# Kernel optimization log

Measured on AMD Instinct MI355X. Metric: run time of the kernel, lower is better.

## Reference

```python
import jax, jax.numpy as jnp
import numpy as np

B, L = 128, 200
NUM_C, D, M = 10000, 128, 64


def setup_inputs() -> dict:
    key = jax.random.key(0)
    ks = jax.random.split(key, 16)
    n = lambda k, s, sc=0.05: jax.random.normal(k, s, dtype=jnp.float32) * sc
    return {
        "q": jax.random.randint(ks[0], (B, L), 0, NUM_C),
        "r": jax.random.randint(ks[1], (B, L), 0, 2),
        "k_emb": n(ks[2], (NUM_C, D)),
        "v_emb": n(ks[3], (2, D)),
        "Mk": n(ks[4], (M, D), 0.2),   # kaiming_normal_
        "Mv0": n(ks[5], (M, D), 0.2),  # kaiming_normal_
        "f_W": n(ks[6], (D, 2 * D)), "f_b": jnp.zeros((D,), jnp.float32),
        "e_W": n(ks[7], (D, D)), "e_b": jnp.zeros((D,), jnp.float32),
        "a_W": n(ks[8], (D, D)), "a_b": jnp.zeros((D,), jnp.float32),
        "ab_W": n(ks[9], (1, D)), "ab_b": jnp.zeros((1,), jnp.float32),
        "df_W": n(ks[10], (1, D)), "df_b": jnp.zeros((1,), jnp.float32),
    }


def reference(q, r, k_emb, v_emb, Mk, Mv0, f_W, f_b, e_W, e_b, a_W, a_b, ab_W, ab_b, df_W, df_b):
    # Embeddings
    k = k_emb[q]                # [B, L, D] question key embedding
    v = k + v_emb[r]            # [B, L, D] value embedding

    # Attention over memory slots, erase/add gates
    w = jax.nn.softmax(jnp.einsum('bld,md->blm', k, Mk), axis=-1)   # [B, L, M]
    e = jax.nn.sigmoid(jnp.einsum('bld,ed->ble', v, e_W) + e_b)      # erase [B, L, D]
    a = jnp.tanh(jnp.einsum('bld,ed->ble', v, a_W) + a_b)            # add   [B, L, D]

    Mvt0 = jnp.broadcast_to(Mv0[None], (q.shape[0], Mv0.shape[0], Mv0.shape[1]))  # [B, M, D]

    def step(Mvt, inp):
        wt, et, at = inp  # [B,M], [B,D], [B,D]
        # read uses memory BEFORE this timestep's write (Mv[:, :-1] in torch)
        read = jnp.einsum('bm,bmd->bd', wt, Mvt)
        we = wt[:, :, None]
        Mvt_new = Mvt * (1.0 - we * et[:, None, :]) + we * at[:, None, :]
        return Mvt_new, read

    _, reads = jax.lax.scan(
        step, Mvt0,
        (w.transpose(1, 0, 2), e.transpose(1, 0, 2), a.transpose(1, 0, 2)))
    reads = reads.transpose(1, 0, 2)  # [B, L, D]

    f = jnp.tanh(jnp.concatenate([reads, k], axis=-1) @ f_W.T + f_b)  # [B, L, D]
    stu_ability = jnp.tanh(f @ ab_W.T + ab_b)   # [B, L, 1] (dropout is identity in eval)
    que_diff = jnp.tanh(k @ df_W.T + df_b)      # [B, L, 1]
    p = jax.nn.sigmoid(3.0 * stu_ability - que_diff)
    return p.squeeze(-1)  # [B, L]
```

## Files before the change

kernel.cpp:

```cpp
#include <hip/hip_runtime.h>

typedef unsigned short ushort_t;
typedef short bf16x8 __attribute__((ext_vector_type(8)));
typedef float f32x4 __attribute__((ext_vector_type(4)));

#define B_ 128
#define L_ 200
#define D_ 128
#define M_ 64

__device__ __forceinline__ float fast_sigmoid(float x) {
    return 1.f / (1.f + __expf(-x));
}

__device__ __forceinline__ float fast_tanh(float x) {
    float xc = fminf(fmaxf(x, -15.f), 15.f);
    float e = __expf(2.f * xc);
    return (e - 1.f) / (e + 1.f);
}

__device__ __forceinline__ ushort_t f2bf(float f) {
    union { float f; unsigned int u; } x;
    x.f = f;
    unsigned int u = x.u;
    unsigned int r = (u + 0x7FFFu + ((u >> 16) & 1u)) >> 16;
    return (ushort_t)r;
}

__device__ __forceinline__ uint4 pack8(float4 a, float4 b) {
    uint4 u;
    u.x = (unsigned)f2bf(a.x) | ((unsigned)f2bf(a.y) << 16);
    u.y = (unsigned)f2bf(a.z) | ((unsigned)f2bf(a.w) << 16);
    u.z = (unsigned)f2bf(b.x) | ((unsigned)f2bf(b.y) << 16);
    u.w = (unsigned)f2bf(b.z) | ((unsigned)f2bf(b.w) << 16);
    return u;
}

#define F_WQ   0u
#define F_EAQ  1638400u
#define F_FKQ  8192000u
#define F_RD   11468800u
#define F_DIFF 14745600u
#define F_PACK 14771200u
#define WPACK_N 57344
#define FPACK_N 16384

__global__ __launch_bounds__(256) void k_pack(
    const float* __restrict__ Mk, const float* __restrict__ eW,
    const float* __restrict__ aW, const float* __restrict__ fW,
    ushort_t* __restrict__ Wpack, ushort_t* __restrict__ Fpack)
{
    int i = blockIdx.x * 256 + threadIdx.x;
    if (i < WPACK_N) {
        int g = i >> 9, lane = (i >> 3) & 63, j = i & 7;
        int nt = g >> 2, ks = g & 3;
        int col = nt * 16 + (lane & 15);
        int d = ks * 32 + ((lane >> 4) << 3) + j;
        float v;
        if (col < 64)       v = Mk[col * 128 + d];
        else if (col < 192) v = eW[(col - 64) * 128 + d];
        else if (col < 320) v = aW[(col - 192) * 128 + d];
        else                v = fW[(col - 320) * 256 + 128 + d];
        Wpack[i] = f2bf(v);
    } else if (i < WPACK_N + FPACK_N) {
        int e = i - WPACK_N;
        int g = e >> 9, lane = (e >> 3) & 63, j = e & 7;
        int nt = g >> 2, ks = g & 3;
        int col = nt * 16 + (lane & 15);
        int d = ks * 32 + ((lane >> 4) << 3) + j;
        Fpack[e] = f2bf(fW[col * 256 + d]);
    }
}

__device__ __forceinline__ void loadB4(const ushort_t* __restrict__ base,
                                       int nt, int lane, bf16x8* b) {
    const ushort_t* p = base + (nt * 256 + lane) * 8;
    b[0] = *(const bf16x8*)(p);
    b[1] = *(const bf16x8*)(p + 512);
    b[2] = *(const bf16x8*)(p + 1024);
    b[3] = *(const bf16x8*)(p + 1536);
}

__global__ __launch_bounds__(256) void k_pre_mfma(
    const int* __restrict__ q, const int* __restrict__ r,
    const float* __restrict__ k_emb, const float* __restrict__ v_emb,
    const ushort_t* __restrict__ Wpack,
    const float* __restrict__ e_b, const float* __restrict__ a_b,
    const float* __restrict__ df_W, const float* __restrict__ df_b,
    float* __restrict__ wq, float* __restrict__ eaq,
    float* __restrict__ fkq, float* __restrict__ diffq)
{
    __shared__ ushort_t sA[8192];
    __shared__ float slog[64 * 68];

    const int tid = threadIdx.x;
    const int pos0 = (blockIdx.x >> 1) * 64;
    const int ng = blockIdx.x & 1;
    const int wave = tid >> 6;
    const int lane = tid & 63;

    #pragma unroll
    for (int i = 0; i < 4; i++) {
        int E = tid + 256 * i;
        int mtile = E >> 8, ks = (E >> 6) & 3, le = E & 63;
        int prow = pos0 + mtile * 16 + (le & 15);
        int dof = ks * 32 + ((le >> 4) << 3);
        int qv = q[prow];
        const float4* kp = (const float4*)(k_emb + qv * 128 + dof);
        float4 ka = kp[0], kb = kp[1];
        if (ng == 0) {
            *(uint4*)&sA[E * 8] = pack8(ka, kb);
        } else {
            int rv = r[prow];
            const float4* vp = (const float4*)(v_emb + rv * 128 + dof);
            float4 va = vp[0], vb = vp[1];
            float4 s0, s1;
            s0.x = ka.x + va.x; s0.y = ka.y + va.y; s0.z = ka.z + va.z; s0.w = ka.w + va.w;
            s1.x = kb.x + vb.x; s1.y = kb.y + vb.y; s1.z = kb.z + vb.z; s1.w = kb.w + vb.w;
            *(uint4*)&sA[E * 8] = pack8(s0, s1);
        }
    }
    __syncthreads();

    bf16x8 A[4];
    #pragma unroll
    for (int ks = 0; ks < 4; ks++)
        A[ks] = *(bf16x8*)&sA[((wave * 4 + ks) * 64 + lane) * 8];

    const int col = lane & 15;
    const int quad = lane >> 4;
    const int rbase = wave * 16 + quad * 4;

    if (ng == 0) {
        bf16x8 Bb[2][4];
        loadB4(Wpack, 0, lane, Bb[0]);
        #pragma unroll
        for (int j = 0; j < 12; j++) {
            if (j < 11) {
                int jn = j + 1;
                loadB4(Wpack, (jn < 4) ? jn : jn + 16, lane, Bb[jn & 1]);
            }
            f32x4 acc = {0.f, 0.f, 0.f, 0.f};
            #pragma unroll
            for (int ks = 0; ks < 4; ks++)
                acc = __builtin_amdgcn_mfma_f32_16x16x32_bf16(A[ks], Bb[j & 1][ks], acc, 0, 0, 0);
            if (j < 4) {
                #pragma unroll
                for (int reg = 0; reg < 4; reg++)
                    slog[(rbase + reg) * 68 + j * 16 + col] = acc[reg];
            } else {
                int c = (j - 4) * 16 + col;
                #pragma unroll
                for (int reg = 0; reg < 4; reg++)
                    fkq[(pos0 + rbase + reg) * 128 + c] = acc[reg];
            }
        }

        {
            int row = tid >> 2, ln = tid & 3;
            int pos = pos0 + row;
            int qv = q[pos];
            const float4* kp = (const float4*)(k_emb + qv * 128) + ln * 8;
            const float4* dfp = (const float4*)df_W + ln * 8;
            float s = 0.f;
            #pragma unroll
            for (int j = 0; j < 8; j++) {
                float4 a = kp[j], b = dfp[j];
                s = fmaf(a.x, b.x, fmaf(a.y, b.y, fmaf(a.z, b.z, fmaf(a.w, b.w, s))));
            }
            s += __shfl_xor(s, 1); s += __shfl_xor(s, 2);
            if (ln == 0) diffq[pos] = fast_tanh(s + df_b[0]);
        }

        __syncthreads();

        {
            int row = tid >> 2, ln = tid & 3;
            const float* lr = slog + row * 68 + ln * 16;
            float v[16];
            #pragma unroll
            for (int j = 0; j < 16; j++) v[j] = lr[j];
            float mx = v[0];
            #pragma unroll
            for (int j = 1; j < 16; j++) mx = fmaxf(mx, v[j]);
            mx = fmaxf(mx, __shfl_xor(mx, 1));
            mx = fmaxf(mx, __shfl_xor(mx, 2));
            float s = 0.f;
            #pragma unroll
            for (int j = 0; j < 16; j++) { v[j] = __expf(v[j] - mx); s += v[j]; }
            s += __shfl_xor(s, 1); s += __shfl_xor(s, 2);
            float inv = 1.f / s;
            float* wout = wq + (pos0 + row) * 64 + ln * 16;
            #pragma unroll
            for (int j = 0; j < 16; j++) wout[j] = v[j] * inv;
        }
    } else {
        bf16x8 Be[2][4], Ba[2][4];
        loadB4(Wpack, 4, lane, Be[0]);
        loadB4(Wpack, 12, lane, Ba[0]);
        #pragma unroll
        for (int i = 0; i < 8; i++) {
            if (i < 7) {
                loadB4(Wpack, 5 + i, lane, Be[(i + 1) & 1]);
                loadB4(Wpack, 13 + i, lane, Ba[(i + 1) & 1]);
            }
            f32x4 ae = {0.f, 0.f, 0.f, 0.f};
            f32x4 aa = {0.f, 0.f, 0.f, 0.f};
            #pragma unroll
            for (int ks = 0; ks < 4; ks++) {
                ae = __builtin_amdgcn_mfma_f32_16x16x32_bf16(A[ks], Be[i & 1][ks], ae, 0, 0, 0);
                aa = __builtin_amdgcn_mfma_f32_16x16x32_bf16(A[ks], Ba[i & 1][ks], aa, 0, 0, 0);
            }
            int c = i * 16 + col;
            float ebv = e_b[c], abv = a_b[c];
            #pragma unroll
            for (int reg = 0; reg < 4; reg++) {
                float2 o;
                o.x = fast_sigmoid(ae[reg] + ebv);
                o.y = fast_tanh(aa[reg] + abv);
                *(float2*)(eaq + ((pos0 + rbase + reg) * 128 + c) * 2) = o;
            }
        }
    }
}

__global__ __launch_bounds__(256) void k_scan(
    const float* __restrict__ wq, const float* __restrict__ eaq,
    const float* __restrict__ Mv0, float* __restrict__ reads)
{
    __shared__ float pbuf[2][4][8][64];

    const int tid = threadIdx.x;
    const int b = blockIdx.x >> 1;
    const int dh = blockIdx.x & 1;
    const int sc = __builtin_amdgcn_readfirstlane(tid >> 6);
    const int lane = tid & 63;
    const int d = dh * 64 + lane;

    float Mv[16];
    #pragma unroll
    for (int j = 0; j < 16; j++) Mv[j] = Mv0[(sc * 16 + j) * D_ + d];

    const float4* wbase = (const float4*)(wq + b * (L_ * M_) + sc * 16);
    const float2* eabase = (const float2*)(eaq + b * (L_ * 256)) + d;
    float* rbase = reads + b * (L_ * D_) + dh * 64;

    const int rtt = tid >> 6;
    const int rdd = tid & 63;

    for (int c = 0; c < 25; c++) {
        const int t0 = c * 8;
        const int bb = c & 1;
        #pragma unroll
        for (int tt = 0; tt < 8; tt++) {
            const float4* wp = wbase + (t0 + tt) * 16;
            float4 w0 = wp[0], w1 = wp[1], w2 = wp[2], w3 = wp[3];
            float2 ea = eabase[(t0 + tt) * 128];
            float ev = ea.x, av = ea.y, ne = -ev;
            float r0, r1;
            r0 = w0.x * Mv[0];
            r1 = w0.y * Mv[1];
            r0 = fmaf(w0.z, Mv[2], r0);  r1 = fmaf(w0.w, Mv[3], r1);
            r0 = fmaf(w1.x, Mv[4], r0);  r1 = fmaf(w1.y, Mv[5], r1);
            r0 = fmaf(w1.z, Mv[6], r0);  r1 = fmaf(w1.w, Mv[7], r1);
            r0 = fmaf(w2.x, Mv[8], r0);  r1 = fmaf(w2.y, Mv[9], r1);
            r0 = fmaf(w2.z, Mv[10], r0); r1 = fmaf(w2.w, Mv[11], r1);
            r0 = fmaf(w3.x, Mv[12], r0); r1 = fmaf(w3.y, Mv[13], r1);
            r0 = fmaf(w3.z, Mv[14], r0); r1 = fmaf(w3.w, Mv[15], r1);
            Mv[0]  = fmaf(w0.x, fmaf(ne, Mv[0],  av), Mv[0]);
            Mv[1]  = fmaf(w0.y, fmaf(ne, Mv[1],  av), Mv[1]);
            Mv[2]  = fmaf(w0.z, fmaf(ne, Mv[2],  av), Mv[2]);
            Mv[3]  = fmaf(w0.w, fmaf(ne, Mv[3],  av), Mv[3]);
            Mv[4]  = fmaf(w1.x, fmaf(ne, Mv[4],  av), Mv[4]);
            Mv[5]  = fmaf(w1.y, fmaf(ne, Mv[5],  av), Mv[5]);
            Mv[6]  = fmaf(w1.z, fmaf(ne, Mv[6],  av), Mv[6]);
            Mv[7]  = fmaf(w1.w, fmaf(ne, Mv[7],  av), Mv[7]);
            Mv[8]  = fmaf(w2.x, fmaf(ne, Mv[8],  av), Mv[8]);
            Mv[9]  = fmaf(w2.y, fmaf(ne, Mv[9],  av), Mv[9]);
            Mv[10] = fmaf(w2.z, fmaf(ne, Mv[10], av), Mv[10]);
            Mv[11] = fmaf(w2.w, fmaf(ne, Mv[11], av), Mv[11]);
            Mv[12] = fmaf(w3.x, fmaf(ne, Mv[12], av), Mv[12]);
            Mv[13] = fmaf(w3.y, fmaf(ne, Mv[13], av), Mv[13]);
            Mv[14] = fmaf(w3.z, fmaf(ne, Mv[14], av), Mv[14]);
            Mv[15] = fmaf(w3.w, fmaf(ne, Mv[15], av), Mv[15]);
            pbuf[bb][sc][tt][lane] = r0 + r1;
        }
        __syncthreads();
        {
            float s0 = pbuf[bb][0][rtt][rdd] + pbuf[bb][1][rtt][rdd]
                     + pbuf[bb][2][rtt][rdd] + pbuf[bb][3][rtt][rdd];
            float s1 = pbuf[bb][0][rtt + 4][rdd] + pbuf[bb][1][rtt + 4][rdd]
                     + pbuf[bb][2][rtt + 4][rdd] + pbuf[bb][3][rtt + 4][rdd];
            rbase[(t0 + rtt) * D_ + rdd] = s0;
            rbase[(t0 + rtt + 4) * D_ + rdd] = s1;
        }
    }
}

__global__ __launch_bounds__(512) void k_final_mfma(
    const float* __restrict__ reads, const float* __restrict__ fkq,
    const float* __restrict__ diffq, const ushort_t* __restrict__ Fpack,
    const float* __restrict__ f_b, const float* __restrict__ ab_W,
    const float* __restrict__ ab_b, float* __restrict__ out)
{
    __shared__ ushort_t srA[8192];
    __shared__ float sab[64 * 2];

    const int tid = threadIdx.x;
    const int pos0 = blockIdx.x * 64;
    const int wave = tid >> 6;
    const int lane = tid & 63;
    const int mt = wave & 3;
    const int half = wave >> 2;

    #pragma unroll
    for (int i = 0; i < 2; i++) {
        int E = tid + 512 * i;
        int mtile = E >> 8, ks = (E >> 6) & 3, le = E & 63;
        int prow = pos0 + mtile * 16 + (le & 15);
        int dof = ks * 32 + ((le >> 4) << 3);
        const float4* rp = (const float4*)(reads + prow * 128 + dof);
        *(uint4*)&srA[E * 8] = pack8(rp[0], rp[1]);
    }
    __syncthreads();

    bf16x8 A[4];
    #pragma unroll
    for (int ks = 0; ks < 4; ks++)
        A[ks] = *(bf16x8*)&srA[((mt * 4 + ks) * 64 + lane) * 8];

    const int col = lane & 15;
    const int quad = lane >> 4;
    const int rbase = mt * 16 + quad * 4;

    float abacc[4] = {0.f, 0.f, 0.f, 0.f};

    bf16x8 Bb[2][4];
    loadB4(Fpack, half * 4, lane, Bb[0]);
    #pragma unroll
    for (int i = 0; i < 4; i++) {
        if (i < 3) loadB4(Fpack, half * 4 + i + 1, lane, Bb[(i + 1) & 1]);
        f32x4 acc = {0.f, 0.f, 0.f, 0.f};
        #pragma unroll
        for (int ks = 0; ks < 4; ks++)
            acc = __builtin_amdgcn_mfma_f32_16x16x32_bf16(A[ks], Bb[i & 1][ks], acc, 0, 0, 0);
        int c = (half * 4 + i) * 16 + col;
        float fb = f_b[c];
        float abw = ab_W[c];
        #pragma unroll
        for (int reg = 0; reg < 4; reg++) {
            float fv = fast_tanh(acc[reg] + fkq[(pos0 + rbase + reg) * 128 + c] + fb);
            abacc[reg] = fmaf(abw, fv, abacc[reg]);
        }
    }

    #pragma unroll
    for (int reg = 0; reg < 4; reg++) {
        float v = abacc[reg];
        v += __shfl_xor(v, 1); v += __shfl_xor(v, 2);
        v += __shfl_xor(v, 4); v += __shfl_xor(v, 8);
        abacc[reg] = v;
    }
    if (col == 0) {
        #pragma unroll
        for (int reg = 0; reg < 4; reg++)
            sab[(rbase + reg) * 2 + half] = abacc[reg];
    }
    __syncthreads();
    if (tid < 64) {
        float ab = fast_tanh(sab[tid * 2] + sab[tid * 2 + 1] + ab_b[0]);
        int pos = pos0 + tid;
        out[pos] = fast_sigmoid(3.f * ab - diffq[pos]);
    }
}

extern "C" void kernel_launch(void* const* d_in, const int* in_sizes, int n_in,
                              void* d_out, int out_size, void* d_ws, size_t ws_size,
                              hipStream_t stream)
{
    const int*   q     = (const int*)d_in[0];
    const int*   r     = (const int*)d_in[1];
    const float* k_emb = (const float*)d_in[2];
    const float* v_emb = (const float*)d_in[3];
    const float* Mk    = (const float*)d_in[4];
    const float* Mv0   = (const float*)d_in[5];
    const float* f_W   = (const float*)d_in[6];
    const float* f_b   = (const float*)d_in[7];
    const float* e_W   = (const float*)d_in[8];
    const float* e_b   = (const float*)d_in[9];
    const float* a_W   = (const float*)d_in[10];
    const float* a_b   = (const float*)d_in[11];
    const float* ab_W  = (const float*)d_in[12];
    const float* ab_b  = (const float*)d_in[13];
    const float* df_W  = (const float*)d_in[14];
    const float* df_b  = (const float*)d_in[15];

    float* ws = (float*)d_ws;
    float* out = (float*)d_out;
    ushort_t* Wpack = (ushort_t*)(ws + F_PACK);
    ushort_t* Fpack = Wpack + WPACK_N;

    k_pack<<<288, 256, 0, stream>>>(Mk, e_W, a_W, f_W, Wpack, Fpack);

    k_pre_mfma<<<800, 256, 0, stream>>>(
        q, r, k_emb, v_emb, Wpack, e_b, a_b, df_W, df_b,
        ws + F_WQ, ws + F_EAQ, ws + F_FKQ, ws + F_DIFF);

    k_scan<<<256, 256, 0, stream>>>(
        ws + F_WQ, ws + F_EAQ, Mv0, ws + F_RD);

    k_final_mfma<<<400, 512, 0, stream>>>(
        ws + F_RD, ws + F_FKQ, ws + F_DIFF, Fpack,
        f_b, ab_W, ab_b, out);
}
```

Measured before the change: 160.2 us.

## Split scan across eight slot waves with register prefetch, merge pre-kernel halves

The scan kernel now uses 512 threads, so each of eight waves owns 8 memory slots instead of 16. Weight and gate data for the next 8 timesteps are double-buffered in registers to hide load latency behind the serial recurrence. The pre kernel merges its two half-blocks into one 512-thread block that stages both the key and value tiles, and moves the difficulty dot product onto the value-half waves. The final kernel hoists its fkq loads ahead of the barrier. The cost is higher register pressure and a wider eight-way LDS reduction per step.

New measurement: 151.2 us. 1.06x faster.

```diff
diff --git a/kernel.cpp b/kernel.cpp
--- a/kernel.cpp
+++ b/kernel.cpp
@@ -81,7 +81,7 @@
     b[3] = *(const bf16x8*)(p + 1536);
 }
 
-__global__ __launch_bounds__(256) void k_pre_mfma(
+__global__ __launch_bounds__(512) void k_pre_mfma(
     const int* __restrict__ q, const int* __restrict__ r,
     const float* __restrict__ k_emb, const float* __restrict__ v_emb,
     const ushort_t* __restrict__ Wpack,
@@ -90,48 +90,49 @@
     float* __restrict__ wq, float* __restrict__ eaq,
     float* __restrict__ fkq, float* __restrict__ diffq)
 {
-    __shared__ ushort_t sA[8192];
+    __shared__ ushort_t skA[8192];
+    __shared__ ushort_t svA[8192];
     __shared__ float slog[64 * 68];
 
     const int tid = threadIdx.x;
-    const int pos0 = (blockIdx.x >> 1) * 64;
-    const int ng = blockIdx.x & 1;
+    const int pos0 = blockIdx.x * 64;
     const int wave = tid >> 6;
     const int lane = tid & 63;
-
-    #pragma unroll
-    for (int i = 0; i < 4; i++) {
-        int E = tid + 256 * i;
+    const int mt = wave & 3;
+    const int nh = wave >> 2;
+
+    #pragma unroll
+    for (int i = 0; i < 2; i++) {
+        int E = tid + 512 * i;
         int mtile = E >> 8, ks = (E >> 6) & 3, le = E & 63;
         int prow = pos0 + mtile * 16 + (le & 15);
         int dof = ks * 32 + ((le >> 4) << 3);
-        int qv = q[prow];
+        int qv = q[prow], rv = r[prow];
         const float4* kp = (const float4*)(k_emb + qv * 128 + dof);
         float4 ka = kp[0], kb = kp[1];
-        if (ng == 0) {
-            *(uint4*)&sA[E * 8] = pack8(ka, kb);
-        } else {
-            int rv = r[prow];
-            const float4* vp = (const float4*)(v_emb + rv * 128 + dof);
-            float4 va = vp[0], vb = vp[1];
-            float4 s0, s1;
-            s0.x = ka.x + va.x; s0.y = ka.y + va.y; s0.z = ka.z + va.z; s0.w = ka.w + va.w;
-            s1.x = kb.x + vb.x; s1.y = kb.y + vb.y; s1.z = kb.z + vb.z; s1.w = kb.w + vb.w;
-            *(uint4*)&sA[E * 8] = pack8(s0, s1);
-        }
+        const float4* vp = (const float4*)(v_emb + rv * 128 + dof);
+        float4 va = vp[0], vb = vp[1];
+        *(uint4*)&skA[E * 8] = pack8(ka, kb);
+        float4 s0, s1;
+        s0.x = ka.x + va.x; s0.y = ka.y + va.y; s0.z = ka.z + va.z; s0.w = ka.w + va.w;
+        s1.x = kb.x + vb.x; s1.y = kb.y + vb.y; s1.z = kb.z + vb.z; s1.w = kb.w + vb.w;
+        *(uint4*)&svA[E * 8] = pack8(s0, s1);
     }
     __syncthreads();
 
     bf16x8 A[4];
-    #pragma unroll
-    for (int ks = 0; ks < 4; ks++)
-        A[ks] = *(bf16x8*)&sA[((wave * 4 + ks) * 64 + lane) * 8];
+    {
+        const ushort_t* src = nh ? svA : skA;
+        #pragma unroll
+        for (int ks = 0; ks < 4; ks++)
+            A[ks] = *(const bf16x8*)&src[((mt * 4 + ks) * 64 + lane) * 8];
+    }
 
     const int col = lane & 15;
     const int quad = lane >> 4;
-    const int rbase = wave * 16 + quad * 4;
-
-    if (ng == 0) {
+    const int rbase = mt * 16 + quad * 4;
+
+    if (nh == 0) {
         bf16x8 Bb[2][4];
         loadB4(Wpack, 0, lane, Bb[0]);
         #pragma unroll
@@ -155,25 +156,6 @@
                     fkq[(pos0 + rbase + reg) * 128 + c] = acc[reg];
             }
         }
-
-        {
-            int row = tid >> 2, ln = tid & 3;
-            int pos = pos0 + row;
-            int qv = q[pos];
-            const float4* kp = (const float4*)(k_emb + qv * 128) + ln * 8;
-            const float4* dfp = (const float4*)df_W + ln * 8;
-            float s = 0.f;
-            #pragma unroll
-            for (int j = 0; j < 8; j++) {
-                float4 a = kp[j], b = dfp[j];
-                s = fmaf(a.x, b.x, fmaf(a.y, b.y, fmaf(a.z, b.z, fmaf(a.w, b.w, s))));
-            }
-            s += __shfl_xor(s, 1); s += __shfl_xor(s, 2);
-            if (ln == 0) diffq[pos] = fast_tanh(s + df_b[0]);
-        }
-
-        __syncthreads();
-
         {
             int row = tid >> 2, ln = tid & 3;
             const float* lr = slog + row * 68 + ln * 16;
@@ -221,80 +203,104 @@
                 *(float2*)(eaq + ((pos0 + rbase + reg) * 128 + c) * 2) = o;
             }
         }
-    }
-}
-
-__global__ __launch_bounds__(256) void k_scan(
+        {
+            int t2 = tid - 256;
+            int row = t2 >> 2, ln = t2 & 3;
+            int pos = pos0 + row;
+            int qv = q[pos];
+            const float4* kp = (const float4*)(k_emb + qv * 128) + ln * 8;
+            const float4* dfp = (const float4*)df_W + ln * 8;
+            float s = 0.f;
+            #pragma unroll
+            for (int j = 0; j < 8; j++) {
+                float4 a = kp[j], b = dfp[j];
+                s = fmaf(a.x, b.x, fmaf(a.y, b.y, fmaf(a.z, b.z, fmaf(a.w, b.w, s))));
+            }
+            s += __shfl_xor(s, 1); s += __shfl_xor(s, 2);
+            if (ln == 0) diffq[pos] = fast_tanh(s + df_b[0]);
+        }
+    }
+}
+
+#define SC_PREFETCH(wX, eX, cN)                                            \
+    _Pragma("unroll")                                                      \
+    for (int tt = 0; tt < 8; tt++) {                                       \
+        wX[2 * tt]     = wb4[((cN) * 8 + tt) * 16 + sc * 2];               \
+        wX[2 * tt + 1] = wb4[((cN) * 8 + tt) * 16 + sc * 2 + 1];           \
+        eX[tt]         = eab[((cN) * 8 + tt) * 128];                       \
+    }
+
+#define SC_COMPUTE(wX, eX, bb)                                             \
+    _Pragma("unroll")                                                      \
+    for (int tt = 0; tt < 8; tt++) {                                       \
+        float4 u = wX[2 * tt], v = wX[2 * tt + 1];                         \
+        float2 ea = eX[tt];                                                \
+        float ev = ea.x, av = ea.y, ne = -ev;                              \
+        float r0 = u.x * Mv[0];                                            \
+        float r1 = u.y * Mv[1];                                            \
+        r0 = fmaf(u.z, Mv[2], r0); r1 = fmaf(u.w, Mv[3], r1);              \
+        r0 = fmaf(v.x, Mv[4], r0); r1 = fmaf(v.y, Mv[5], r1);              \
+        r0 = fmaf(v.z, Mv[6], r0); r1 = fmaf(v.w, Mv[7], r1);              \
+        Mv[0] = fmaf(u.x, fmaf(ne, Mv[0], av), Mv[0]);                     \
+        Mv[1] = fmaf(u.y, fmaf(ne, Mv[1], av), Mv[1]);                     \
+        Mv[2] = fmaf(u.z, fmaf(ne, Mv[2], av), Mv[2]);                     \
+        Mv[3] = fmaf(u.w, fmaf(ne, Mv[3], av), Mv[3]);                     \
+        Mv[4] = fmaf(v.x, fmaf(ne, Mv[4], av), Mv[4]);                     \
+        Mv[5] = fmaf(v.y, fmaf(ne, Mv[5], av), Mv[5]);                     \
+        Mv[6] = fmaf(v.z, fmaf(ne, Mv[6], av), Mv[6]);                     \
+        Mv[7] = fmaf(v.w, fmaf(ne, Mv[7], av), Mv[7]);                     \
+        pbuf[bb][sc][tt][lane] = r0 + r1;                                  \
+    }
+
+#define SC_REDUCE(bb, c0) {                                                \
+        float s = pbuf[bb][0][wv][lane] + pbuf[bb][1][wv][lane]            \
+                + pbuf[bb][2][wv][lane] + pbuf[bb][3][wv][lane]            \
+                + pbuf[bb][4][wv][lane] + pbuf[bb][5][wv][lane]            \
+                + pbuf[bb][6][wv][lane] + pbuf[bb][7][wv][lane];           \
+        rbase[((c0) * 8 + wv) * 128 + lane] = s;                           \
+    }
+
+__global__ __launch_bounds__(512, 2) void k_scan(
     const float* __restrict__ wq, const float* __restrict__ eaq,
     const float* __restrict__ Mv0, float* __restrict__ reads)
 {
-    __shared__ float pbuf[2][4][8][64];
+    __shared__ float pbuf[2][8][8][64];
 
     const int tid = threadIdx.x;
     const int b = blockIdx.x >> 1;
     const int dh = blockIdx.x & 1;
-    const int sc = __builtin_amdgcn_readfirstlane(tid >> 6);
+    const int wv = tid >> 6;
+    const int sc = __builtin_amdgcn_readfirstlane(wv);
     const int lane = tid & 63;
     const int d = dh * 64 + lane;
 
-    float Mv[16];
-    #pragma unroll
-    for (int j = 0; j < 16; j++) Mv[j] = Mv0[(sc * 16 + j) * D_ + d];
-
-    const float4* wbase = (const float4*)(wq + b * (L_ * M_) + sc * 16);
-    const float2* eabase = (const float2*)(eaq + b * (L_ * 256)) + d;
+    float Mv[8];
+    #pragma unroll
+    for (int j = 0; j < 8; j++) Mv[j] = Mv0[(sc * 8 + j) * D_ + d];
+
+    const float4* wb4 = (const float4*)(wq + b * (L_ * M_));
+    const float2* eab = (const float2*)eaq + b * (L_ * 128) + d;
     float* rbase = reads + b * (L_ * D_) + dh * 64;
 
-    const int rtt = tid >> 6;
-    const int rdd = tid & 63;
-
-    for (int c = 0; c < 25; c++) {
-        const int t0 = c * 8;
-        const int bb = c & 1;
-        #pragma unroll
-        for (int tt = 0; tt < 8; tt++) {
-            const float4* wp = wbase + (t0 + tt) * 16;
-            float4 w0 = wp[0], w1 = wp[1], w2 = wp[2], w3 = wp[3];
-            float2 ea = eabase[(t0 + tt) * 128];
-            float ev = ea.x, av = ea.y, ne = -ev;
-            float r0, r1;
-            r0 = w0.x * Mv[0];
-            r1 = w0.y * Mv[1];
-            r0 = fmaf(w0.z, Mv[2], r0);  r1 = fmaf(w0.w, Mv[3], r1);
-            r0 = fmaf(w1.x, Mv[4], r0);  r1 = fmaf(w1.y, Mv[5], r1);
-            r0 = fmaf(w1.z, Mv[6], r0);  r1 = fmaf(w1.w, Mv[7], r1);
-            r0 = fmaf(w2.x, Mv[8], r0);  r1 = fmaf(w2.y, Mv[9], r1);
-            r0 = fmaf(w2.z, Mv[10], r0); r1 = fmaf(w2.w, Mv[11], r1);
-            r0 = fmaf(w3.x, Mv[12], r0); r1 = fmaf(w3.y, Mv[13], r1);
-            r0 = fmaf(w3.z, Mv[14], r0); r1 = fmaf(w3.w, Mv[15], r1);
-            Mv[0]  = fmaf(w0.x, fmaf(ne, Mv[0],  av), Mv[0]);
-            Mv[1]  = fmaf(w0.y, fmaf(ne, Mv[1],  av), Mv[1]);
-            Mv[2]  = fmaf(w0.z, fmaf(ne, Mv[2],  av), Mv[2]);
-            Mv[3]  = fmaf(w0.w, fmaf(ne, Mv[3],  av), Mv[3]);
-            Mv[4]  = fmaf(w1.x, fmaf(ne, Mv[4],  av), Mv[4]);
-            Mv[5]  = fmaf(w1.y, fmaf(ne, Mv[5],  av), Mv[5]);
-            Mv[6]  = fmaf(w1.z, fmaf(ne, Mv[6],  av), Mv[6]);
-            Mv[7]  = fmaf(w1.w, fmaf(ne, Mv[7],  av), Mv[7]);
-            Mv[8]  = fmaf(w2.x, fmaf(ne, Mv[8],  av), Mv[8]);
-            Mv[9]  = fmaf(w2.y, fmaf(ne, Mv[9],  av), Mv[9]);
-            Mv[10] = fmaf(w2.z, fmaf(ne, Mv[10], av), Mv[10]);
-            Mv[11] = fmaf(w2.w, fmaf(ne, Mv[11], av), Mv[11]);
-            Mv[12] = fmaf(w3.x, fmaf(ne, Mv[12], av), Mv[12]);
-            Mv[13] = fmaf(w3.y, fmaf(ne, Mv[13], av), Mv[13]);
-            Mv[14] = fmaf(w3.z, fmaf(ne, Mv[14], av), Mv[14]);
-            Mv[15] = fmaf(w3.w, fmaf(ne, Mv[15], av), Mv[15]);
-            pbuf[bb][sc][tt][lane] = r0 + r1;
-        }
+    float4 wA[16], wB[16];
+    float2 eA[8], eB[8];
+
+    SC_PREFETCH(wA, eA, 0);
+
+    for (int cc = 0; cc < 12; cc++) {
+        const int c0 = 2 * cc;
+        SC_PREFETCH(wB, eB, c0 + 1);
+        SC_COMPUTE(wA, eA, 0);
         __syncthreads();
-        {
-            float s0 = pbuf[bb][0][rtt][rdd] + pbuf[bb][1][rtt][rdd]
-                     + pbuf[bb][2][rtt][rdd] + pbuf[bb][3][rtt][rdd];
-            float s1 = pbuf[bb][0][rtt + 4][rdd] + pbuf[bb][1][rtt + 4][rdd]
-                     + pbuf[bb][2][rtt + 4][rdd] + pbuf[bb][3][rtt + 4][rdd];
-            rbase[(t0 + rtt) * D_ + rdd] = s0;
-            rbase[(t0 + rtt + 4) * D_ + rdd] = s1;
-        }
-    }
+        SC_REDUCE(0, c0);
+        SC_PREFETCH(wA, eA, c0 + 2);
+        SC_COMPUTE(wB, eB, 1);
+        __syncthreads();
+        SC_REDUCE(1, c0 + 1);
+    }
+    SC_COMPUTE(wA, eA, 0);
+    __syncthreads();
+    SC_REDUCE(0, 24);
 }
 
 __global__ __launch_bounds__(512) void k_final_mfma(
@@ -322,16 +328,24 @@
         const float4* rp = (const float4*)(reads + prow * 128 + dof);
         *(uint4*)&srA[E * 8] = pack8(rp[0], rp[1]);
     }
-    __syncthreads();
-
-    bf16x8 A[4];
-    #pragma unroll
-    for (int ks = 0; ks < 4; ks++)
-        A[ks] = *(bf16x8*)&srA[((mt * 4 + ks) * 64 + lane) * 8];
 
     const int col = lane & 15;
     const int quad = lane >> 4;
     const int rbase = mt * 16 + quad * 4;
+
+    float fkv[16];
+    #pragma unroll
+    for (int i = 0; i < 4; i++)
+        #pragma unroll
+        for (int reg = 0; reg < 4; reg++)
+            fkv[i * 4 + reg] = fkq[(pos0 + rbase + reg) * 128 + (half * 4 + i) * 16 + col];
+
+    __syncthreads();
+
+    bf16x8 A[4];
+    #pragma unroll
+    for (int ks = 0; ks < 4; ks++)
+        A[ks] = *(const bf16x8*)&srA[((mt * 4 + ks) * 64 + lane) * 8];
 
     float abacc[4] = {0.f, 0.f, 0.f, 0.f};
 
@@ -349,7 +363,7 @@
         float abw = ab_W[c];
         #pragma unroll
         for (int reg = 0; reg < 4; reg++) {
-            float fv = fast_tanh(acc[reg] + fkq[(pos0 + rbase + reg) * 128 + c] + fb);
+            float fv = fast_tanh(acc[reg] + fkv[i * 4 + reg] + fb);
             abacc[reg] = fmaf(abw, fv, abacc[reg]);
         }
     }
@@ -402,11 +416,11 @@
 
     k_pack<<<288, 256, 0, stream>>>(Mk, e_W, a_W, f_W, Wpack, Fpack);
 
-    k_pre_mfma<<<800, 256, 0, stream>>>(
+    k_pre_mfma<<<400, 512, 0, stream>>>(
         q, r, k_emb, v_emb, Wpack, e_b, a_b, df_W, df_b,
         ws + F_WQ, ws + F_EAQ, ws + F_FKQ, ws + F_DIFF);
 
-    k_scan<<<256, 256, 0, stream>>>(
+    k_scan<<<256, 512, 0, stream>>>(
         ws + F_WQ, ws + F_EAQ, Mv0, ws + F_RD);
 
     k_final_mfma<<<400, 512, 0, stream>>>(
```

## Merge pre-kernel halves, shuffle-reduce scan reads into packed bf16 MFMA layout

Applied to the files above, without the earlier changes.

The pre-processing kernel now handles both the key and value GEMM halves in one 512-thread block that shares the gathered embeddings. The question-difficulty dot product is computed from the staged bf16 keys by the second half of the threads. The scan kernel drops its shared-memory partial buffer and per-8-step barriers: each wave covers 16 d-columns across four slot groups and reduces with warp shuffles. It then writes the reads directly as bf16 in the MFMA A-operand layout, so the final kernel loads A fragments without an LDS staging pass. The intent is to cut barriers and LDS traffic in the serial scan and to remove the conversion and staging step in the final kernel. The cost is more shuffles per timestep, scattered 2-byte stores, and bf16 rounding in the difficulty dot product.

Measured after the change: 224.0 us. 1.4x slower.

```diff
diff --git a/kernel.cpp b/kernel.cpp
--- a/kernel.cpp
+++ b/kernel.cpp
@@ -17,6 +17,12 @@
     float xc = fminf(fmaxf(x, -15.f), 15.f);
     float e = __expf(2.f * xc);
     return (e - 1.f) / (e + 1.f);
+}
+
+__device__ __forceinline__ float bf2f(ushort_t h) {
+    union { unsigned int u; float f; } x;
+    x.u = ((unsigned int)h) << 16;
+    return x.f;
 }
 
 __device__ __forceinline__ ushort_t f2bf(float f) {
@@ -81,7 +87,7 @@
     b[3] = *(const bf16x8*)(p + 1536);
 }
 
-__global__ __launch_bounds__(256) void k_pre_mfma(
+__global__ __launch_bounds__(512) void k_pre_mfma(
     const int* __restrict__ q, const int* __restrict__ r,
     const float* __restrict__ k_emb, const float* __restrict__ v_emb,
     const ushort_t* __restrict__ Wpack,
@@ -90,48 +96,49 @@
     float* __restrict__ wq, float* __restrict__ eaq,
     float* __restrict__ fkq, float* __restrict__ diffq)
 {
-    __shared__ ushort_t sA[8192];
+    __shared__ ushort_t skA[8192];
+    __shared__ ushort_t svA[8192];
     __shared__ float slog[64 * 68];
 
     const int tid = threadIdx.x;
-    const int pos0 = (blockIdx.x >> 1) * 64;
-    const int ng = blockIdx.x & 1;
+    const int pos0 = blockIdx.x * 64;
     const int wave = tid >> 6;
     const int lane = tid & 63;
+    const int mt = wave & 3;
+    const int nh = wave >> 2;
 
     #pragma unroll
-    for (int i = 0; i < 4; i++) {
-        int E = tid + 256 * i;
+    for (int i = 0; i < 2; i++) {
+        int E = tid + 512 * i;
         int mtile = E >> 8, ks = (E >> 6) & 3, le = E & 63;
         int prow = pos0 + mtile * 16 + (le & 15);
         int dof = ks * 32 + ((le >> 4) << 3);
-        int qv = q[prow];
+        int qv = q[prow], rv = r[prow];
         const float4* kp = (const float4*)(k_emb + qv * 128 + dof);
         float4 ka = kp[0], kb = kp[1];
-        if (ng == 0) {
-            *(uint4*)&sA[E * 8] = pack8(ka, kb);
-        } else {
-            int rv = r[prow];
-            const float4* vp = (const float4*)(v_emb + rv * 128 + dof);
-            float4 va = vp[0], vb = vp[1];
-            float4 s0, s1;
-            s0.x = ka.x + va.x; s0.y = ka.y + va.y; s0.z = ka.z + va.z; s0.w = ka.w + va.w;
-            s1.x = kb.x + vb.x; s1.y = kb.y + vb.y; s1.z = kb.z + vb.z; s1.w = kb.w + vb.w;
-            *(uint4*)&sA[E * 8] = pack8(s0, s1);
-        }
+        const float4* vp = (const float4*)(v_emb + rv * 128 + dof);
+        float4 va = vp[0], vb = vp[1];
+        *(uint4*)&skA[E * 8] = pack8(ka, kb);
+        float4 s0, s1;
+        s0.x = ka.x + va.x; s0.y = ka.y + va.y; s0.z = ka.z + va.z; s0.w = ka.w + va.w;
+        s1.x = kb.x + vb.x; s1.y = kb.y + vb.y; s1.z = kb.z + vb.z; s1.w = kb.w + vb.w;
+        *(uint4*)&svA[E * 8] = pack8(s0, s1);
     }
     __syncthreads();
 
     bf16x8 A[4];
-    #pragma unroll
-    for (int ks = 0; ks < 4; ks++)
-        A[ks] = *(bf16x8*)&sA[((wave * 4 + ks) * 64 + lane) * 8];
+    {
+        const ushort_t* src = nh ? svA : skA;
+        #pragma unroll
+        for (int ks = 0; ks < 4; ks++)
+            A[ks] = *(const bf16x8*)&src[((mt * 4 + ks) * 64 + lane) * 8];
+    }
 
     const int col = lane & 15;
     const int quad = lane >> 4;
-    const int rbase = wave * 16 + quad * 4;
-
-    if (ng == 0) {
+    const int rbase = mt * 16 + quad * 4;
+
+    if (nh == 0) {
         bf16x8 Bb[2][4];
         loadB4(Wpack, 0, lane, Bb[0]);
         #pragma unroll
@@ -155,25 +162,6 @@
                     fkq[(pos0 + rbase + reg) * 128 + c] = acc[reg];
             }
         }
-
-        {
-            int row = tid >> 2, ln = tid & 3;
-            int pos = pos0 + row;
-            int qv = q[pos];
-            const float4* kp = (const float4*)(k_emb + qv * 128) + ln * 8;
-            const float4* dfp = (const float4*)df_W + ln * 8;
-            float s = 0.f;
-            #pragma unroll
-            for (int j = 0; j < 8; j++) {
-                float4 a = kp[j], b = dfp[j];
-                s = fmaf(a.x, b.x, fmaf(a.y, b.y, fmaf(a.z, b.z, fmaf(a.w, b.w, s))));
-            }
-            s += __shfl_xor(s, 1); s += __shfl_xor(s, 2);
-            if (ln == 0) diffq[pos] = fast_tanh(s + df_b[0]);
-        }
-
-        __syncthreads();
-
         {
             int row = tid >> 2, ln = tid & 3;
             const float* lr = slog + row * 68 + ln * 16;
@@ -221,89 +209,100 @@
                 *(float2*)(eaq + ((pos0 + rbase + reg) * 128 + c) * 2) = o;
             }
         }
+        {
+            int t2 = tid - 256;
+            int row = t2 >> 2, ks = t2 & 3;
+            int mtile = row >> 4, rowin = row & 15;
+            float s = 0.f;
+            #pragma unroll
+            for (int q8 = 0; q8 < 4; q8++) {
+                bf16x8 kv = *(const bf16x8*)&skA[((mtile * 4 + ks) * 64 + (q8 * 16 + rowin)) * 8];
+                const float* dfp = df_W + ks * 32 + q8 * 8;
+                #pragma unroll
+                for (int j = 0; j < 8; j++)
+                    s = fmaf(bf2f((ushort_t)kv[j]), dfp[j], s);
+            }
+            s += __shfl_xor(s, 1); s += __shfl_xor(s, 2);
+            if (ks == 0) diffq[pos0 + row] = fast_tanh(s + df_b[0]);
+        }
     }
 }
 
 __global__ __launch_bounds__(256) void k_scan(
     const float* __restrict__ wq, const float* __restrict__ eaq,
-    const float* __restrict__ Mv0, float* __restrict__ reads)
+    const float* __restrict__ Mv0, ushort_t* __restrict__ rdpack)
 {
-    __shared__ float pbuf[2][4][8][64];
-
     const int tid = threadIdx.x;
     const int b = blockIdx.x >> 1;
     const int dh = blockIdx.x & 1;
-    const int sc = __builtin_amdgcn_readfirstlane(tid >> 6);
+    const int wv = tid >> 6;
     const int lane = tid & 63;
-    const int d = dh * 64 + lane;
+    const int s = lane >> 4;
+    const int dl = lane & 15;
+    const int d = dh * 64 + wv * 16 + dl;
 
     float Mv[16];
     #pragma unroll
-    for (int j = 0; j < 16; j++) Mv[j] = Mv0[(sc * 16 + j) * D_ + d];
-
-    const float4* wbase = (const float4*)(wq + b * (L_ * M_) + sc * 16);
-    const float2* eabase = (const float2*)(eaq + b * (L_ * 256)) + d;
-    float* rbase = reads + b * (L_ * D_) + dh * 64;
-
-    const int rtt = tid >> 6;
-    const int rdd = tid & 63;
-
-    for (int c = 0; c < 25; c++) {
-        const int t0 = c * 8;
-        const int bb = c & 1;
-        #pragma unroll
-        for (int tt = 0; tt < 8; tt++) {
-            const float4* wp = wbase + (t0 + tt) * 16;
-            float4 w0 = wp[0], w1 = wp[1], w2 = wp[2], w3 = wp[3];
-            float2 ea = eabase[(t0 + tt) * 128];
-            float ev = ea.x, av = ea.y, ne = -ev;
-            float r0, r1;
-            r0 = w0.x * Mv[0];
-            r1 = w0.y * Mv[1];
-            r0 = fmaf(w0.z, Mv[2], r0);  r1 = fmaf(w0.w, Mv[3], r1);
-            r0 = fmaf(w1.x, Mv[4], r0);  r1 = fmaf(w1.y, Mv[5], r1);
-            r0 = fmaf(w1.z, Mv[6], r0);  r1 = fmaf(w1.w, Mv[7], r1);
-            r0 = fmaf(w2.x, Mv[8], r0);  r1 = fmaf(w2.y, Mv[9], r1);
-            r0 = fmaf(w2.z, Mv[10], r0); r1 = fmaf(w2.w, Mv[11], r1);
-            r0 = fmaf(w3.x, Mv[12], r0); r1 = fmaf(w3.y, Mv[13], r1);
-            r0 = fmaf(w3.z, Mv[14], r0); r1 = fmaf(w3.w, Mv[15], r1);
-            Mv[0]  = fmaf(w0.x, fmaf(ne, Mv[0],  av), Mv[0]);
-            Mv[1]  = fmaf(w0.y, fmaf(ne, Mv[1],  av), Mv[1]);
-            Mv[2]  = fmaf(w0.z, fmaf(ne, Mv[2],  av), Mv[2]);
-            Mv[3]  = fmaf(w0.w, fmaf(ne, Mv[3],  av), Mv[3]);
-            Mv[4]  = fmaf(w1.x, fmaf(ne, Mv[4],  av), Mv[4]);
-            Mv[5]  = fmaf(w1.y, fmaf(ne, Mv[5],  av), Mv[5]);
-            Mv[6]  = fmaf(w1.z, fmaf(ne, Mv[6],  av), Mv[6]);
-            Mv[7]  = fmaf(w1.w, fmaf(ne, Mv[7],  av), Mv[7]);
-            Mv[8]  = fmaf(w2.x, fmaf(ne, Mv[8],  av), Mv[8]);
-            Mv[9]  = fmaf(w2.y, fmaf(ne, Mv[9],  av), Mv[9]);
-            Mv[10] = fmaf(w2.z, fmaf(ne, Mv[10], av), Mv[10]);
-            Mv[11] = fmaf(w2.w, fmaf(ne, Mv[11], av), Mv[11]);
-            Mv[12] = fmaf(w3.x, fmaf(ne, Mv[12], av), Mv[12]);
-            Mv[13] = fmaf(w3.y, fmaf(ne, Mv[13], av), Mv[13]);
-            Mv[14] = fmaf(w3.z, fmaf(ne, Mv[14], av), Mv[14]);
-            Mv[15] = fmaf(w3.w, fmaf(ne, Mv[15], av), Mv[15]);
-            pbuf[bb][sc][tt][lane] = r0 + r1;
-        }
-        __syncthreads();
-        {
-            float s0 = pbuf[bb][0][rtt][rdd] + pbuf[bb][1][rtt][rdd]
-                     + pbuf[bb][2][rtt][rdd] + pbuf[bb][3][rtt][rdd];
-            float s1 = pbuf[bb][0][rtt + 4][rdd] + pbuf[bb][1][rtt + 4][rdd]
-                     + pbuf[bb][2][rtt + 4][rdd] + pbuf[bb][3][rtt + 4][rdd];
-            rbase[(t0 + rtt) * D_ + rdd] = s0;
-            rbase[(t0 + rtt + 4) * D_ + rdd] = s1;
+    for (int j = 0; j < 16; j++) Mv[j] = Mv0[(s * 16 + j) * D_ + d];
+
+    const float4* wb4 = (const float4*)(wq + b * (L_ * M_)) + s * 4;
+    const float2* eab = (const float2*)eaq + b * (L_ * 128) + d;
+
+    const int pos_base = b * L_;
+    const int ksd = d >> 5;
+    const int q8d = (d >> 3) & 3;
+    const int jd = d & 7;
+
+    #pragma unroll 2
+    for (int t = 0; t < L_; t++) {
+        const float4* wp = wb4 + t * 16;
+        float4 w0 = wp[0], w1 = wp[1], w2 = wp[2], w3 = wp[3];
+        float2 ea = eab[t * 128];
+        float ev = ea.x, av = ea.y, ne = -ev;
+        float r0, r1, r2, r3;
+        r0 = w0.x * Mv[0];
+        r1 = w0.y * Mv[1];
+        r2 = w0.z * Mv[2];
+        r3 = w0.w * Mv[3];
+        r0 = fmaf(w1.x, Mv[4], r0);  r1 = fmaf(w1.y, Mv[5], r1);
+        r2 = fmaf(w1.z, Mv[6], r2);  r3 = fmaf(w1.w, Mv[7], r3);
+        r0 = fmaf(w2.x, Mv[8], r0);  r1 = fmaf(w2.y, Mv[9], r1);
+        r2 = fmaf(w2.z, Mv[10], r2); r3 = fmaf(w2.w, Mv[11], r3);
+        r0 = fmaf(w3.x, Mv[12], r0); r1 = fmaf(w3.y, Mv[13], r1);
+        r2 = fmaf(w3.z, Mv[14], r2); r3 = fmaf(w3.w, Mv[15], r3);
+        Mv[0]  = fmaf(w0.x, fmaf(ne, Mv[0],  av), Mv[0]);
+        Mv[1]  = fmaf(w0.y, fmaf(ne, Mv[1],  av), Mv[1]);
+        Mv[2]  = fmaf(w0.z, fmaf(ne, Mv[2],  av), Mv[2]);
+        Mv[3]  = fmaf(w0.w, fmaf(ne, Mv[3],  av), Mv[3]);
+        Mv[4]  = fmaf(w1.x, fmaf(ne, Mv[4],  av), Mv[4]);
+        Mv[5]  = fmaf(w1.y, fmaf(ne, Mv[5],  av), Mv[5]);
+        Mv[6]  = fmaf(w1.z, fmaf(ne, Mv[6],  av), Mv[6]);
+        Mv[7]  = fmaf(w1.w, fmaf(ne, Mv[7],  av), Mv[7]);
+        Mv[8]  = fmaf(w2.x, fmaf(ne, Mv[8],  av), Mv[8]);
+        Mv[9]  = fmaf(w2.y, fmaf(ne, Mv[9],  av), Mv[9]);
+        Mv[10] = fmaf(w2.z, fmaf(ne, Mv[10], av), Mv[10]);
+        Mv[11] = fmaf(w2.w, fmaf(ne, Mv[11], av), Mv[11]);
+        Mv[12] = fmaf(w3.x, fmaf(ne, Mv[12], av), Mv[12]);
+        Mv[13] = fmaf(w3.y, fmaf(ne, Mv[13], av), Mv[13]);
+        Mv[14] = fmaf(w3.z, fmaf(ne, Mv[14], av), Mv[14]);
+        Mv[15] = fmaf(w3.w, fmaf(ne, Mv[15], av), Mv[15]);
+        float rd = (r0 + r1) + (r2 + r3);
+        rd += __shfl_xor(rd, 16);
+        rd += __shfl_xor(rd, 32);
+        if (s == 0) {
+            int pos = pos_base + t;
+            int idx = (((pos >> 4) * 4 + ksd) * 64 + (q8d * 16 + (pos & 15))) * 8 + jd;
+            rdpack[idx] = f2bf(rd);
         }
     }
 }
 
 __global__ __launch_bounds__(512) void k_final_mfma(
-    const float* __restrict__ reads, const float* __restrict__ fkq,
+    const ushort_t* __restrict__ rdpack, const float* __restrict__ fkq,
     const float* __restrict__ diffq, const ushort_t* __restrict__ Fpack,
     const float* __restrict__ f_b, const float* __restrict__ ab_W,
     const float* __restrict__ ab_b, float* __restrict__ out)
 {
-    __shared__ ushort_t srA[8192];
     __shared__ float sab[64 * 2];
 
     const int tid = threadIdx.x;
@@ -313,25 +312,24 @@
     const int mt = wave & 3;
     const int half = wave >> 2;
 
-    #pragma unroll
-    for (int i = 0; i < 2; i++) {
-        int E = tid + 512 * i;
-        int mtile = E >> 8, ks = (E >> 6) & 3, le = E & 63;
-        int prow = pos0 + mtile * 16 + (le & 15);
-        int dof = ks * 32 + ((le >> 4) << 3);
-        const float4* rp = (const float4*)(reads + prow * 128 + dof);
-        *(uint4*)&srA[E * 8] = pack8(rp[0], rp[1]);
-    }
-    __syncthreads();
-
-    bf16x8 A[4];
-    #pragma unroll
-    for (int ks = 0; ks < 4; ks++)
-        A[ks] = *(bf16x8*)&srA[((mt * 4 + ks) * 64 + lane) * 8];
-
     const int col = lane & 15;
     const int quad = lane >> 4;
     const int rbase = mt * 16 + quad * 4;
+
+    bf16x8 A[4];
+    {
+        const ushort_t* rp = rdpack + (blockIdx.x * 4 + mt) * 2048 + lane * 8;
+        #pragma unroll
+        for (int ks = 0; ks < 4; ks++)
+            A[ks] = *(const bf16x8*)(rp + ks * 512);
+    }
+
+    float fkv[16];
+    #pragma unroll
+    for (int i = 0; i < 4; i++)
+        #pragma unroll
+        for (int reg = 0; reg < 4; reg++)
+            fkv[i * 4 + reg] = fkq[(pos0 + rbase + reg) * 128 + (half * 4 + i) * 16 + col];
 
     float abacc[4] = {0.f, 0.f, 0.f, 0.f};
 
@@ -349,7 +347,7 @@
         float abw = ab_W[c];
         #pragma unroll
         for (int reg = 0; reg < 4; reg++) {
-            float fv = fast_tanh(acc[reg] + fkq[(pos0 + rbase + reg) * 128 + c] + fb);
+            float fv = fast_tanh(acc[reg] + fkv[i * 4 + reg] + fb);
             abacc[reg] = fmaf(abw, fv, abacc[reg]);
         }
     }
@@ -399,17 +397,18 @@
     float* out = (float*)d_out;
     ushort_t* Wpack = (ushort_t*)(ws + F_PACK);
     ushort_t* Fpack = Wpack + WPACK_N;
+    ushort_t* rdpack = (ushort_t*)(ws + F_RD);
 
     k_pack<<<288, 256, 0, stream>>>(Mk, e_W, a_W, f_W, Wpack, Fpack);
 
-    k_pre_mfma<<<800, 256, 0, stream>>>(
+    k_pre_mfma<<<400, 512, 0, stream>>>(
         q, r, k_emb, v_emb, Wpack, e_b, a_b, df_W, df_b,
         ws + F_WQ, ws + F_EAQ, ws + F_FKQ, ws + F_DIFF);
 
     k_scan<<<256, 256, 0, stream>>>(
-        ws + F_WQ, ws + F_EAQ, Mv0, ws + F_RD);
+        ws + F_WQ, ws + F_EAQ, Mv0, rdpack);
 
     k_final_mfma<<<400, 512, 0, stream>>>(
-        ws + F_RD, ws + F_FKQ, ws + F_DIFF, Fpack,
+        rdpack, ws + F_FKQ, ws + F_DIFF, Fpack,
         f_b, ab_W, ab_b, out);
 }
```
